# Performance work log

Hardware: AMD Instinct MI355X
Metric: run time of the kernel (lower is better)

## Reference

```python
import jax, jax.numpy as jnp
import numpy as np

B, T, E, H = 8, 2048, 1024, 128

def setup_inputs() -> dict:
    key = jax.random.key(0)
    k1, k2, k3, k4 = jax.random.split(key, 4)
    s = 0.02
    return {
        "x":  jax.random.normal(k1, (B, T, E), dtype=jnp.float32),
        "Wq": jax.random.normal(k2, (E, H), dtype=jnp.float32) * s,
        "Wk": jax.random.normal(k3, (E, H), dtype=jnp.float32) * s,
        "Wv": jax.random.normal(k4, (E, H), dtype=jnp.float32) * s,
    }

def reference(x, Wq, Wk, Wv):
    # q,k,v: [B,T,H]
    q = jnp.einsum("bte,eh->bth", x, Wq)
    k = jnp.einsum("bte,eh->bth", x, Wk)
    v = jnp.einsum("bte,eh->bth", x, Wv)
    scale = jnp.asarray(q.shape[-1], q.dtype) ** -0.5
    wei = jnp.einsum("bqh,bkh->bqk", q, k) * scale  # [B,T,T]
    causal = jnp.tril(jnp.ones((wei.shape[1], wei.shape[2]), dtype=bool))
    wei = jnp.where(causal, wei, jnp.asarray(-jnp.inf, wei.dtype))
    wei = jax.nn.softmax(wei, axis=-1)
    # dropout_prob = 0.0 -> identity
    return jnp.einsum("bqk,bkh->bqh", wei, v)
```

## Files before the change

### kernel.cpp

```cpp
#include <hip/hip_runtime.h>

#define BB 8
#define TT 2048
#define EE 1024
#define HH 128

typedef __bf16 bf16;
typedef __attribute__((ext_vector_type(8))) __bf16 bf16x8;
typedef __attribute__((ext_vector_type(4))) __bf16 bf16x4;
typedef __attribute__((ext_vector_type(4))) float f32x4;
typedef __attribute__((ext_vector_type(16))) float f32x16;

__device__ __host__ inline int qb_off(int qb) {
  int h = qb >> 1;
  return qb + h * (h - 1) + ((qb & 1) ? h : 0);
}
#define NSLAB 72

__device__ inline void gload_lds16(const bf16* g, bf16* l) {
  __builtin_amdgcn_global_load_lds((const __attribute__((address_space(1))) unsigned int*)g,
                                   (__attribute__((address_space(3))) unsigned int*)l,
                                   16, 0, 0);
}

__global__ __launch_bounds__(256) void wt_kernel(const float* __restrict__ wq,
                                                 const float* __restrict__ wk,
                                                 const float* __restrict__ wv,
                                                 bf16* __restrict__ wt) {
  __shared__ float tile[64][65];
  const int z = blockIdx.z;
  const float* w = (z == 0) ? wq : ((z == 1) ? wk : wv);
  const int k0 = blockIdx.x * 64;
  const int h0 = blockIdx.y * 64;
  const int c = threadIdx.x & 63;
  const int r0 = threadIdx.x >> 6;
#pragma unroll
  for (int i = 0; i < 16; ++i) {
    int tt = r0 + i * 4;
    tile[tt][c] = w[(size_t)(k0 + tt) * HH + h0 + c];
  }
  __syncthreads();
#pragma unroll
  for (int i = 0; i < 16; ++i) {
    int hh = r0 + i * 4;
    wt[((size_t)(z * HH + h0 + hh)) * EE + k0 + c] = (bf16)tile[c][hh];
  }
}

__global__ __launch_bounds__(256) void xcvt_kernel(const float* __restrict__ x,
                                                   bf16* __restrict__ xb) {
  const size_t base = (size_t)blockIdx.x * 4096 + threadIdx.x * 4;
#pragma unroll
  for (int j = 0; j < 4; ++j) {
    size_t idx = base + j * 1024;
    f32x4 xv = *(const f32x4*)(x + idx);
    bf16x4 xo;
#pragma unroll
    for (int i = 0; i < 4; ++i) xo[i] = (bf16)xv[i];
    *(bf16x4*)(xb + idx) = xo;
  }
}

__global__ __launch_bounds__(256) void gemm_kernel(const bf16* __restrict__ xb,
                                                   const bf16* __restrict__ wt,
                                                   bf16* __restrict__ q,
                                                   bf16* __restrict__ k,
                                                   bf16* __restrict__ v) {
  __shared__ bf16 As[128 * 32];
  __shared__ bf16 Bs[96 * 32];
  const int tid = threadIdx.x;
  const int lane = tid & 63;
  const int wave = tid >> 6;
  const int l16 = lane & 15;
  const int quad = lane >> 4;
  const int wm = wave & 1;
  const int wn = wave >> 1;
  const int bm = blockIdx.x;
  const int ntile = blockIdx.y;

  const int trow = tid >> 2;
  const int tsub = (tid & 3) * 8;
  const bf16* gA = xb + (size_t)(bm * 128 + trow) * EE + tsub;
  const bf16* gB = wt + (size_t)(ntile * 96 + trow) * EE + tsub;

  f32x4 acc[4][3];
#pragma unroll
  for (int rg = 0; rg < 4; ++rg)
#pragma unroll
    for (int nt = 0; nt < 3; ++nt) acc[rg][nt] = f32x4{0.f, 0.f, 0.f, 0.f};

  for (int ks = 0; ks < EE / 32; ++ks) {
    gload_lds16(gA + ks * 32, &As[wave * 512]);
    gload_lds16(gA + (size_t)64 * EE + ks * 32, &As[2048 + wave * 512]);
    gload_lds16(gB + ks * 32, &Bs[wave * 512]);
    if (tid < 128)
      gload_lds16(gB + (size_t)64 * EE + ks * 32, &Bs[2048 + wave * 512]);
    __syncthreads();

    bf16x8 af[4], bf[3];
#pragma unroll
    for (int rg = 0; rg < 4; ++rg)
      af[rg] = *(const bf16x8*)&As[(wm * 64 + rg * 16 + l16) * 32 + quad * 8];
#pragma unroll
    for (int nt = 0; nt < 3; ++nt)
      bf[nt] = *(const bf16x8*)&Bs[(wn * 48 + nt * 16 + l16) * 32 + quad * 8];
#pragma unroll
    for (int rg = 0; rg < 4; ++rg)
#pragma unroll
      for (int nt = 0; nt < 3; ++nt)
        acc[rg][nt] = __builtin_amdgcn_mfma_f32_16x16x32_bf16(af[rg], bf[nt], acc[rg][nt], 0, 0, 0);
    __syncthreads();
  }

  bf16* outp[3] = {q, k, v};
#pragma unroll
  for (int rg = 0; rg < 4; ++rg)
#pragma unroll
    for (int nt = 0; nt < 3; ++nt) {
      int col = ntile * 96 + wn * 48 + nt * 16 + l16;
      int z = col >> 7;
      int n = col & 127;
#pragma unroll
      for (int r = 0; r < 4; ++r) {
        int row = bm * 128 + wm * 64 + rg * 16 + quad * 4 + r;
        outp[z][(size_t)row * HH + n] = (bf16)acc[rg][nt][r];
      }
    }
}

__global__ __launch_bounds__(256) void vtrans_kernel(const bf16* __restrict__ v,
                                                     bf16* __restrict__ vt) {
  __shared__ bf16 tile[64][65];
  const int b = blockIdx.x;
  const int t0 = blockIdx.y * 64;
  const int h0 = blockIdx.z * 64;
  const int c = threadIdx.x & 63;
  const int r0 = threadIdx.x >> 6;
#pragma unroll
  for (int i = 0; i < 16; ++i) {
    int tt = r0 + i * 4;
    tile[tt][c] = v[((size_t)(b * TT + t0 + tt)) * HH + h0 + c];
  }
  __syncthreads();
#pragma unroll
  for (int i = 0; i < 16; ++i) {
    int hh = r0 + i * 4;
    vt[((size_t)(b * HH + h0 + hh)) * TT + t0 + c] = tile[c][hh];
  }
}


__device__ __forceinline__ unsigned pk2(float a, float b) {
  union { __bf16 h[2]; unsigned u; } x;
  x.h[0] = (__bf16)a;
  x.h[1] = (__bf16)b;
  return x.u;
}

__device__ __forceinline__ void plswap(unsigned& a, unsigned& b) {
  asm volatile("v_permlane32_swap_b32 %0, %1" : "+v"(a), "+v"(b));
}

__device__ __forceinline__ void fbody(const bf16* __restrict__ kp0,
                                      const bf16* __restrict__ vp0,
                                      const bf16x8 (&qf)[8],
                                      bf16x8 (&kf)[8], bf16x8 (&kfn)[8],
                                      f32x16 (&O)[4], float& L,
                                      int k32, int k32n, int kdiag,
                                      int qrow, int hi) {
  const float c_ = 0.12753257680406733f;
  bf16x8 vf[2][4];
#pragma unroll
  for (int s16 = 0; s16 < 2; ++s16)
#pragma unroll
    for (int ht = 0; ht < 4; ++ht)
      vf[s16][ht] = *(const bf16x8*)(vp0 + (size_t)ht * 32 * TT + k32 * 32 + s16 * 16);

  f32x16 S;
#pragma unroll
  for (int r = 0; r < 16; ++r) S[r] = 0.f;
  __builtin_amdgcn_s_setprio(1);
#pragma unroll
  for (int h16 = 0; h16 < 8; ++h16)
    S = __builtin_amdgcn_mfma_f32_32x32x16_bf16(kf[h16], qf[h16], S, 0, 0, 0);
  __builtin_amdgcn_s_setprio(0);

#pragma unroll
  for (int h16 = 0; h16 < 8; ++h16)
    kfn[h16] = *(const bf16x8*)(kp0 + (size_t)k32n * 32 * HH + h16 * 16);

  float p[16];
  if (k32 == kdiag) {
    const int kkb = k32 * 32 + 4 * hi;
#pragma unroll
    for (int r = 0; r < 16; ++r) {
      int kk = kkb + (r & 3) + 8 * (r >> 2);
      float pv = (kk <= qrow) ? exp2f(S[r] * c_) : 0.f;
      p[r] = pv;
      L += pv;
    }
  } else {
#pragma unroll
    for (int r = 0; r < 16; ++r) {
      float pv = exp2f(S[r] * c_);
      p[r] = pv;
      L += pv;
    }
  }

#pragma unroll
  for (int s16 = 0; s16 < 2; ++s16) {
    unsigned w0 = pk2(p[s16 * 8 + 0], p[s16 * 8 + 1]);
    unsigned w1 = pk2(p[s16 * 8 + 2], p[s16 * 8 + 3]);
    unsigned w2 = pk2(p[s16 * 8 + 4], p[s16 * 8 + 5]);
    unsigned w3 = pk2(p[s16 * 8 + 6], p[s16 * 8 + 7]);
    plswap(w0, w2);
    plswap(w1, w3);
    union { unsigned u[4]; bf16x8 v; } af;
    af.u[0] = w0;
    af.u[1] = w1;
    af.u[2] = w2;
    af.u[3] = w3;
    __builtin_amdgcn_s_setprio(1);
#pragma unroll
    for (int ht = 0; ht < 4; ++ht)
      O[ht] = __builtin_amdgcn_mfma_f32_32x32x16_bf16(af.v, vf[s16][ht], O[ht], 0, 0, 0);
    __builtin_amdgcn_s_setprio(0);
  }
}

__global__ __launch_bounds__(256, 2) void flash_kernel(const bf16* __restrict__ q,
                                                       const bf16* __restrict__ k,
                                                       const bf16* __restrict__ vt,
                                                       bf16* __restrict__ opart,
                                                       float* __restrict__ lpart) {
  const int b = blockIdx.x & 7;
  int j = (NSLAB - 1) - (blockIdx.x >> 3);
  int qb = 0, ns = 1;
  while (j >= ns) { j -= ns; ++qb; ns = ((2 * qb + 1) >> 2) + 1; }
  const int s = j;
  const int kt0 = s * 4;
  const int kt1 = min(kt0 + 3, 2 * qb + 1);

  const int lane = threadIdx.x & 63;
  const int wave = threadIdx.x >> 6;
  const int l32 = lane & 31;
  const int hi = lane >> 5;
  const int wrow0 = qb * 128 + wave * 32;
  const int qrow = wrow0 + l32;

  bf16x8 qf[8];
  {
    const bf16* qp = q + (size_t)(b * TT + qrow) * HH + hi * 8;
#pragma unroll
    for (int h16 = 0; h16 < 8; ++h16) qf[h16] = *(const bf16x8*)(qp + h16 * 16);
  }

  f32x16 O[4];
#pragma unroll
  for (int ht = 0; ht < 4; ++ht)
#pragma unroll
    for (int r = 0; r < 16; ++r) O[ht][r] = 0.f;
  float L = 0.f;

  const int kdiag = qb * 4 + wave;
  const int k32b = kt0 * 2;
  const int k32e = min(kt1 * 2 + 1, kdiag);

  const bf16* kp0 = k + ((size_t)b * TT + l32) * HH + hi * 8;
  const bf16* vp0 = vt + ((size_t)b * HH + l32) * TT + hi * 8;

  bf16x8 kfA[8], kfB[8];
#pragma unroll
  for (int h16 = 0; h16 < 8; ++h16)
    kfA[h16] = *(const bf16x8*)(kp0 + (size_t)k32b * 32 * HH + h16 * 16);

  for (int k32 = k32b; k32 <= k32e; k32 += 2) {
    fbody(kp0, vp0, qf, kfA, kfB, O, L, k32, min(k32 + 1, k32e), kdiag, qrow, hi);
    if (k32 + 1 <= k32e)
      fbody(kp0, vp0, qf, kfB, kfA, O, L, k32 + 1, min(k32 + 2, k32e), kdiag, qrow, hi);
  }

  L += __shfl_xor(L, 32, 64);

  const size_t slab = (size_t)(b * NSLAB + qb_off(qb) + s);
  bf16* op = opart + slab * (128 * 128) + (size_t)wave * 32 * 128;
#pragma unroll
  for (int ht = 0; ht < 4; ++ht)
#pragma unroll
    for (int r = 0; r < 16; ++r) {
      int qr = (r & 3) + 8 * (r >> 2) + 4 * hi;
      op[qr * 128 + ht * 32 + l32] = (bf16)O[ht][r];
    }
  if (hi == 0) lpart[slab * 128 + wave * 32 + l32] = L;
}

__global__ __launch_bounds__(128) void combine_kernel(const bf16* __restrict__ opart,
                                                      const float* __restrict__ lpart,
                                                      float* __restrict__ out) {
  const int b = blockIdx.x;
  const int qt16 = blockIdx.y;
  const int half = blockIdx.z;
  const int row = threadIdx.x >> 3;
  const int colo = (threadIdx.x & 7) * 8 + half * 64;
  const int qb = qt16 >> 3;
  const int srow = (qt16 & 7) * 16 + row;
  const int ns = ((2 * qb + 1) >> 2) + 1;
  const size_t slab0 = (size_t)(b * NSLAB + qb_off(qb));

  float acc[8];
#pragma unroll
  for (int j = 0; j < 8; ++j) acc[j] = 0.f;
  float L = 0.f;

  int s = 0;
  for (; s + 4 <= ns; s += 4) {
    float l0 = lpart[(slab0 + s + 0) * 128 + srow];
    float l1 = lpart[(slab0 + s + 1) * 128 + srow];
    float l2 = lpart[(slab0 + s + 2) * 128 + srow];
    float l3 = lpart[(slab0 + s + 3) * 128 + srow];
    bf16x8 v0 = *(const bf16x8*)(opart + (slab0 + s + 0) * (128 * 128) + srow * 128 + colo);
    bf16x8 v1 = *(const bf16x8*)(opart + (slab0 + s + 1) * (128 * 128) + srow * 128 + colo);
    bf16x8 v2 = *(const bf16x8*)(opart + (slab0 + s + 2) * (128 * 128) + srow * 128 + colo);
    bf16x8 v3 = *(const bf16x8*)(opart + (slab0 + s + 3) * (128 * 128) + srow * 128 + colo);
    L += (l0 + l1) + (l2 + l3);
#pragma unroll
    for (int j = 0; j < 8; ++j)
      acc[j] += ((float)v0[j] + (float)v1[j]) + ((float)v2[j] + (float)v3[j]);
  }
  for (; s < ns; ++s) {
    L += lpart[(slab0 + s) * 128 + srow];
    bf16x8 ov = *(const bf16x8*)(opart + (slab0 + s) * (128 * 128) + srow * 128 + colo);
#pragma unroll
    for (int j = 0; j < 8; ++j) acc[j] += (float)ov[j];
  }
  float invL = 1.f / L;
  float* o = out + ((size_t)(b * TT + qt16 * 16 + row)) * HH + colo;
  f32x4 o0, o1;
#pragma unroll
  for (int j = 0; j < 4; ++j) { o0[j] = acc[j] * invL; o1[j] = acc[j + 4] * invL; }
  *(f32x4*)o = o0;
  *(f32x4*)(o + 4) = o1;
}

extern "C" void kernel_launch(void* const* d_in, const int* in_sizes, int n_in,
                              void* d_out, int out_size, void* d_ws, size_t ws_size,
                              hipStream_t stream) {
  const float* x = (const float*)d_in[0];
  const float* wq = (const float*)d_in[1];
  const float* wk = (const float*)d_in[2];
  const float* wv = (const float*)d_in[3];
  float* out = (float*)d_out;

  char* ws = (char*)d_ws;
  const size_t NE = (size_t)BB * TT * HH;
  bf16* wt = (bf16*)ws;
  bf16* xb = (bf16*)(ws + (1 << 20));
  bf16* q = (bf16*)(ws + (33 << 20));
  bf16* k = q + NE;
  bf16* v = k + NE;
  bf16* vt = v + NE;
  bf16* opart = xb;
  float* lpart = (float*)(opart + (size_t)(BB * NSLAB) * 128 * 128);

  wt_kernel<<<dim3(16, 2, 3), 256, 0, stream>>>(wq, wk, wv, wt);
  xcvt_kernel<<<dim3(4096), 256, 0, stream>>>(x, xb);
  gemm_kernel<<<dim3(128, 4), 256, 0, stream>>>(xb, wt, q, k, v);
  vtrans_kernel<<<dim3(8, 32, 2), 256, 0, stream>>>(v, vt);
  flash_kernel<<<dim3(576), 256, 0, stream>>>(q, k, vt, opart, lpart);
  combine_kernel<<<dim3(8, 128, 2), 128, 0, stream>>>(opart, lpart, out);
}
```

Before: 186.3 us.

## Stage K and V tiles in swizzled LDS shared across waves

Replaces per-wave direct global loads of K and V (with register double-buffering of K) with block-cooperative global_load_lds copies of 64-key K and V tiles into XOR-swizzled shared memory. The four waves then read MFMA fragments from LDS. This removes the 4x redundant global/L2 traffic, since every wave previously fetched the same K/V. In exchange it adds two barriers per tile, drops the register prefetch overlap of the next K tile, and uses 32KB of LDS per block.

```diff
diff --git a/kernel.cpp b/kernel.cpp
--- a/kernel.cpp
+++ b/kernel.cpp
@@ -161,79 +161,14 @@
   asm volatile("v_permlane32_swap_b32 %0, %1" : "+v"(a), "+v"(b));
 }
 
-__device__ __forceinline__ void fbody(const bf16* __restrict__ kp0,
-                                      const bf16* __restrict__ vp0,
-                                      const bf16x8 (&qf)[8],
-                                      bf16x8 (&kf)[8], bf16x8 (&kfn)[8],
-                                      f32x16 (&O)[4], float& L,
-                                      int k32, int k32n, int kdiag,
-                                      int qrow, int hi) {
-  const float c_ = 0.12753257680406733f;
-  bf16x8 vf[2][4];
-#pragma unroll
-  for (int s16 = 0; s16 < 2; ++s16)
-#pragma unroll
-    for (int ht = 0; ht < 4; ++ht)
-      vf[s16][ht] = *(const bf16x8*)(vp0 + (size_t)ht * 32 * TT + k32 * 32 + s16 * 16);
-
-  f32x16 S;
-#pragma unroll
-  for (int r = 0; r < 16; ++r) S[r] = 0.f;
-  __builtin_amdgcn_s_setprio(1);
-#pragma unroll
-  for (int h16 = 0; h16 < 8; ++h16)
-    S = __builtin_amdgcn_mfma_f32_32x32x16_bf16(kf[h16], qf[h16], S, 0, 0, 0);
-  __builtin_amdgcn_s_setprio(0);
-
-#pragma unroll
-  for (int h16 = 0; h16 < 8; ++h16)
-    kfn[h16] = *(const bf16x8*)(kp0 + (size_t)k32n * 32 * HH + h16 * 16);
-
-  float p[16];
-  if (k32 == kdiag) {
-    const int kkb = k32 * 32 + 4 * hi;
-#pragma unroll
-    for (int r = 0; r < 16; ++r) {
-      int kk = kkb + (r & 3) + 8 * (r >> 2);
-      float pv = (kk <= qrow) ? exp2f(S[r] * c_) : 0.f;
-      p[r] = pv;
-      L += pv;
-    }
-  } else {
-#pragma unroll
-    for (int r = 0; r < 16; ++r) {
-      float pv = exp2f(S[r] * c_);
-      p[r] = pv;
-      L += pv;
-    }
-  }
-
-#pragma unroll
-  for (int s16 = 0; s16 < 2; ++s16) {
-    unsigned w0 = pk2(p[s16 * 8 + 0], p[s16 * 8 + 1]);
-    unsigned w1 = pk2(p[s16 * 8 + 2], p[s16 * 8 + 3]);
-    unsigned w2 = pk2(p[s16 * 8 + 4], p[s16 * 8 + 5]);
-    unsigned w3 = pk2(p[s16 * 8 + 6], p[s16 * 8 + 7]);
-    plswap(w0, w2);
-    plswap(w1, w3);
-    union { unsigned u[4]; bf16x8 v; } af;
-    af.u[0] = w0;
-    af.u[1] = w1;
-    af.u[2] = w2;
-    af.u[3] = w3;
-    __builtin_amdgcn_s_setprio(1);
-#pragma unroll
-    for (int ht = 0; ht < 4; ++ht)
-      O[ht] = __builtin_amdgcn_mfma_f32_32x32x16_bf16(af.v, vf[s16][ht], O[ht], 0, 0, 0);
-    __builtin_amdgcn_s_setprio(0);
-  }
-}
-
 __global__ __launch_bounds__(256, 2) void flash_kernel(const bf16* __restrict__ q,
                                                        const bf16* __restrict__ k,
                                                        const bf16* __restrict__ vt,
                                                        bf16* __restrict__ opart,
                                                        float* __restrict__ lpart) {
+  __shared__ bf16 Ks[64 * 128];
+  __shared__ bf16 Vs[128 * 64];
+
   const int b = blockIdx.x & 7;
   int j = (NSLAB - 1) - (blockIdx.x >> 3);
   int qb = 0, ns = 1;
@@ -242,12 +177,13 @@
   const int kt0 = s * 4;
   const int kt1 = min(kt0 + 3, 2 * qb + 1);
 
-  const int lane = threadIdx.x & 63;
-  const int wave = threadIdx.x >> 6;
+  const int tid = threadIdx.x;
+  const int lane = tid & 63;
+  const int wave = tid >> 6;
   const int l32 = lane & 31;
   const int hi = lane >> 5;
-  const int wrow0 = qb * 128 + wave * 32;
-  const int qrow = wrow0 + l32;
+  const int qrow = qb * 128 + wave * 32 + l32;
+  const int kdiag = qb * 4 + wave;
 
   bf16x8 qf[8];
   {
@@ -263,22 +199,92 @@
     for (int r = 0; r < 16; ++r) O[ht][r] = 0.f;
   float L = 0.f;
 
-  const int kdiag = qb * 4 + wave;
-  const int k32b = kt0 * 2;
-  const int k32e = min(kt1 * 2 + 1, kdiag);
-
-  const bf16* kp0 = k + ((size_t)b * TT + l32) * HH + hi * 8;
-  const bf16* vp0 = vt + ((size_t)b * HH + l32) * TT + hi * 8;
-
-  bf16x8 kfA[8], kfB[8];
-#pragma unroll
-  for (int h16 = 0; h16 < 8; ++h16)
-    kfA[h16] = *(const bf16x8*)(kp0 + (size_t)k32b * 32 * HH + h16 * 16);
-
-  for (int k32 = k32b; k32 <= k32e; k32 += 2) {
-    fbody(kp0, vp0, qf, kfA, kfB, O, L, k32, min(k32 + 1, k32e), kdiag, qrow, hi);
-    if (k32 + 1 <= k32e)
-      fbody(kp0, vp0, qf, kfB, kfA, O, L, k32 + 1, min(k32 + 2, k32e), kdiag, qrow, hi);
+  const int krow_s = tid >> 4;
+  const int kchk_s = (tid & 15) ^ (krow_s & 7);
+  const int vrow_s = tid >> 3;
+  const int vchk_s = (tid & 7) ^ (vrow_s & 7);
+  const bf16* kg = k + (size_t)b * TT * HH;
+  const bf16* vg = vt + (size_t)b * HH * TT;
+
+  const int kxor = (l32 & 7) << 3;
+  const float c_ = 0.12753257680406733f;
+
+  for (int kt = kt0; kt <= kt1; ++kt) {
+#pragma unroll
+    for (int i = 0; i < 4; ++i)
+      gload_lds16(kg + (size_t)(kt * 64 + i * 16 + krow_s) * HH + kchk_s * 8,
+                  &Ks[(i * 256 + wave * 64) * 8]);
+#pragma unroll
+    for (int i = 0; i < 4; ++i)
+      gload_lds16(vg + (size_t)(i * 32 + vrow_s) * TT + kt * 64 + vchk_s * 8,
+                  &Vs[(i * 256 + wave * 64) * 8]);
+    __syncthreads();
+
+#pragma unroll
+    for (int khalf = 0; khalf < 2; ++khalf) {
+      const int k32 = kt * 2 + khalf;
+      if (k32 <= kdiag) {
+        const bf16* kls = &Ks[(khalf * 32 + l32) * 128];
+        bf16x8 kf[8];
+#pragma unroll
+        for (int h16 = 0; h16 < 8; ++h16)
+          kf[h16] = *(const bf16x8*)&kls[(h16 * 16 + hi * 8) ^ kxor];
+
+        f32x16 S;
+#pragma unroll
+        for (int r = 0; r < 16; ++r) S[r] = 0.f;
+        __builtin_amdgcn_s_setprio(1);
+#pragma unroll
+        for (int h16 = 0; h16 < 8; ++h16)
+          S = __builtin_amdgcn_mfma_f32_32x32x16_bf16(kf[h16], qf[h16], S, 0, 0, 0);
+        __builtin_amdgcn_s_setprio(0);
+
+        float p[16];
+        if (k32 == kdiag) {
+          const int kkb = k32 * 32 + 4 * hi;
+#pragma unroll
+          for (int r = 0; r < 16; ++r) {
+            int kk = kkb + (r & 3) + 8 * (r >> 2);
+            float pv = (kk <= qrow) ? exp2f(S[r] * c_) : 0.f;
+            p[r] = pv;
+            L += pv;
+          }
+        } else {
+#pragma unroll
+          for (int r = 0; r < 16; ++r) {
+            float pv = exp2f(S[r] * c_);
+            p[r] = pv;
+            L += pv;
+          }
+        }
+
+#pragma unroll
+        for (int s16 = 0; s16 < 2; ++s16) {
+          unsigned w0 = pk2(p[s16 * 8 + 0], p[s16 * 8 + 1]);
+          unsigned w1 = pk2(p[s16 * 8 + 2], p[s16 * 8 + 3]);
+          unsigned w2 = pk2(p[s16 * 8 + 4], p[s16 * 8 + 5]);
+          unsigned w3 = pk2(p[s16 * 8 + 6], p[s16 * 8 + 7]);
+          plswap(w0, w2);
+          plswap(w1, w3);
+          union { unsigned u[4]; bf16x8 v; } af;
+          af.u[0] = w0;
+          af.u[1] = w1;
+          af.u[2] = w2;
+          af.u[3] = w3;
+          bf16x8 vf[4];
+#pragma unroll
+          for (int ht = 0; ht < 4; ++ht)
+            vf[ht] = *(const bf16x8*)&Vs[(l32 + 32 * ht) * 64 +
+                                         ((khalf * 32 + s16 * 16 + hi * 8) ^ kxor)];
+          __builtin_amdgcn_s_setprio(1);
+#pragma unroll
+          for (int ht = 0; ht < 4; ++ht)
+            O[ht] = __builtin_amdgcn_mfma_f32_32x32x16_bf16(af.v, vf[ht], O[ht], 0, 0, 0);
+          __builtin_amdgcn_s_setprio(0);
+        }
+      }
+    }
+    __syncthreads();
   }
 
   L += __shfl_xor(L, 32, 64);
```

New measurement: 158.0 us. -15.2%, faster.
